# Optimization experiments

Hardware: AMD Instinct MI355X
Metric: run time of the kernel (lower is better)

## Reference

```python
import jax, jax.numpy as jnp
import numpy as np

B, S, D, H = 4, 2048, 512, 8
DEPTH = D // H


def setup_inputs() -> dict:
    key = jax.random.key(0)
    ks = jax.random.split(key, 12)
    s = 0.02
    return {
        "q": jax.random.normal(ks[0], (B, S, D), jnp.float32),
        "k": jax.random.normal(ks[1], (B, S, D), jnp.float32),
        "v": jax.random.normal(ks[2], (B, S, D), jnp.float32),
        "mask": jax.random.randint(ks[3], (B, 1, 1, S), 0, 2, jnp.int32),
        "wq": jax.random.normal(ks[4], (D, D), jnp.float32) * s,
        "bq": jnp.zeros((D,), jnp.float32),
        "wk": jax.random.normal(ks[5], (D, D), jnp.float32) * s,
        "bk": jnp.zeros((D,), jnp.float32),
        "wv": jax.random.normal(ks[6], (D, D), jnp.float32) * s,
        "bv": jnp.zeros((D,), jnp.float32),
        "wo": jax.random.normal(ks[7], (D, D), jnp.float32) * s,
        "bo": jnp.zeros((D,), jnp.float32),
    }


def _split_heads(x):
    # [B,S,D] -> [B,H,S,depth]
    b = x.shape[0]
    return x.reshape(b, -1, H, DEPTH).transpose(0, 2, 1, 3)


def reference(q, k, v, mask, wq, bq, wk, bk, wv, bv, wo, bo):
    qh = _split_heads(q @ wq + bq)
    kh = _split_heads(k @ wk + bk)
    vh = _split_heads(v @ wv + bv)
    scale = 1.0 / jnp.sqrt(jnp.float32(DEPTH))
    logits = jnp.einsum("bhqd,bhkd->bhqk", qh, kh) * scale
    logits = logits + mask.astype(jnp.float32) * -1e9
    attn = jax.nn.softmax(logits, axis=-1)  # [B,H,Sq,Sk]
    out = jnp.einsum("bhqk,bhkd->bhqd", attn, vh)
    out = out.transpose(0, 2, 1, 3).reshape(q.shape[0], -1, D)
    out = out @ wo + bo
    return out, attn
```

## Files before the change

### kernel.cpp

```cpp
#include <hip/hip_runtime.h>

#define B_ 4
#define S_ 2048
#define D_ 512
#define H_ 8
#define DP_ 64
#define NT_ (S_/64)

typedef __attribute__((ext_vector_type(4))) float f32x4;
typedef __attribute__((ext_vector_type(8))) short short8;

__device__ __forceinline__ short f2bf(float f){
  unsigned u = __float_as_uint(f);
  u += 0x7fff + ((u >> 16) & 1);
  return (short)(u >> 16);
}

#define SWZ(r, kb) ((r)*64 + ((kb) ^ (((r)&7)<<3)))

template<int NC>
__device__ __forceinline__ void stage_tile(const short* __restrict__ g, int rowStride,
                                           short* shbase, int w, int l){
  #pragma unroll
  for(int i = 0; i < NC; ++i){
    int byte = (w*NC + i)*1024 + l*16;
    int row = byte >> 7;
    int gs = ((byte >> 4) & 7) ^ (row & 7);
    const short* src = g + (size_t)row*rowStride + gs*8;
    __builtin_amdgcn_global_load_lds((const __attribute__((address_space(1))) void*)src,
        (__attribute__((address_space(3))) void*)(shbase + (w*NC + i)*512), 16, 0, 0);
  }
}

__global__ void k_prep(const float* __restrict__ w0, const float* __restrict__ w1,
                       const float* __restrict__ w2, const float* __restrict__ w3,
                       short* __restrict__ t0, short* __restrict__ t1,
                       short* __restrict__ t2, short* __restrict__ t3){
  __shared__ float t[32][33];
  const float* w = blockIdx.z == 0 ? w0 : blockIdx.z == 1 ? w1 : blockIdx.z == 2 ? w2 : w3;
  short* wt = blockIdx.z == 0 ? t0 : blockIdx.z == 1 ? t1 : blockIdx.z == 2 ? t2 : t3;
  int bx = blockIdx.x * 32, by = blockIdx.y * 32;
  int tx = threadIdx.x, ty = threadIdx.y;
  #pragma unroll
  for(int i = 0; i < 32; i += 8) t[ty + i][tx] = w[(by + ty + i) * D_ + bx + tx];
  __syncthreads();
  #pragma unroll
  for(int i = 0; i < 32; i += 8) wt[(bx + ty + i) * D_ + by + tx] = f2bf(t[tx][ty + i]);
}

__global__ void k_cast(const float* __restrict__ q, const float* __restrict__ k,
                       const float* __restrict__ v, short* __restrict__ dst){
  const float* s = blockIdx.z == 0 ? q : blockIdx.z == 1 ? k : v;
  short* d = dst + (size_t)blockIdx.z * (B_ * S_ * D_);
  int i = blockIdx.x * 256 + threadIdx.x;
  float4 a = ((const float4*)s)[i * 2];
  float4 b = ((const float4*)s)[i * 2 + 1];
  short8 o;
  o[0]=f2bf(a.x); o[1]=f2bf(a.y); o[2]=f2bf(a.z); o[3]=f2bf(a.w);
  o[4]=f2bf(b.x); o[5]=f2bf(b.y); o[6]=f2bf(b.z); o[7]=f2bf(b.w);
  ((short8*)d)[i] = o;
}

__global__ void k_maskbias(const int* __restrict__ mask, float* __restrict__ mb){
  int i = blockIdx.x * 256 + threadIdx.x;
  if(i < B_ * S_) mb[i] = mask[i] ? -1.0e9f : 0.0f;
}

template<int MODE>
__global__ __launch_bounds__(256) void k_gemm(const short* __restrict__ X,
                                              const short* __restrict__ WT,
                                              const float* __restrict__ bias,
                                              void* __restrict__ Outv){
  __shared__ __align__(16) short As[2][4096];
  __shared__ __align__(16) short Bs[2][4096];
  const int t = threadIdx.x;
  const int m0 = blockIdx.x * 64, n0 = blockIdx.y * 64;
  const int l = t & 63, w = t >> 6;
  const int wr = w >> 1, wc = w & 1;
  f32x4 acc[2][2] = {};
  const short* Xb = X + (size_t)m0 * D_;
  const short* Wb = WT + (size_t)n0 * D_;
  stage_tile<2>(Xb, D_, As[0], w, l);
  stage_tile<2>(Wb, D_, Bs[0], w, l);
  __syncthreads();
  for(int kt = 0; kt < D_ / 64; ++kt){
    if(kt + 1 < D_ / 64){
      stage_tile<2>(Xb + (kt + 1) * 64, D_, As[(kt + 1) & 1], w, l);
      stage_tile<2>(Wb + (kt + 1) * 64, D_, Bs[(kt + 1) & 1], w, l);
    }
    const short* Ac = As[kt & 1];
    const short* Bc = Bs[kt & 1];
    #pragma unroll
    for(int ks = 0; ks < 2; ++ks){
      const int kb = ks * 32 + ((l >> 4) << 3);
      short8 a[2], b[2];
      #pragma unroll
      for(int mt = 0; mt < 2; ++mt){
        int r = wr * 32 + mt * 16 + (l & 15);
        a[mt] = *reinterpret_cast<const short8*>(&Ac[SWZ(r, kb)]);
      }
      #pragma unroll
      for(int nt = 0; nt < 2; ++nt){
        int r = wc * 32 + nt * 16 + (l & 15);
        b[nt] = *reinterpret_cast<const short8*>(&Bc[SWZ(r, kb)]);
      }
      __builtin_amdgcn_s_setprio(1);
      #pragma unroll
      for(int mt = 0; mt < 2; ++mt)
        #pragma unroll
        for(int nt = 0; nt < 2; ++nt)
          acc[mt][nt] = __builtin_amdgcn_mfma_f32_16x16x32_bf16(a[mt], b[nt], acc[mt][nt], 0, 0, 0);
      __builtin_amdgcn_s_setprio(0);
    }
    __syncthreads();
  }
  #pragma unroll
  for(int mt = 0; mt < 2; ++mt){
    #pragma unroll
    for(int nt = 0; nt < 2; ++nt){
      const int n = n0 + wc * 32 + nt * 16 + (l & 15);
      const int m4 = m0 + wr * 32 + mt * 16 + ((l >> 4) << 2);
      float vals[4];
      #pragma unroll
      for(int r = 0; r < 4; ++r) vals[r] = acc[mt][nt][r] + bias[n];
      if(MODE == 0){
        #pragma unroll
        for(int r = 0; r < 4; ++r){
          int m = m4 + r;
          ((short*)Outv)[(((size_t)((m >> 11) * H_ + (n >> 6))) * S_ + (m & 2047)) * DP_ + (n & 63)] = f2bf(vals[r]);
        }
      } else if(MODE == 1){
        #pragma unroll
        for(int r = 0; r < 4; ++r)
          ((float*)Outv)[(size_t)(m4 + r) * D_ + n] = vals[r];
      } else {
        short4 pv4;
        pv4.x = f2bf(vals[0]); pv4.y = f2bf(vals[1]); pv4.z = f2bf(vals[2]); pv4.w = f2bf(vals[3]);
        *reinterpret_cast<short4*>(&((short*)Outv)[
            (((size_t)((m4 >> 11) * H_ + (n >> 6))) * DP_ + (n & 63)) * S_ + (m4 & 2047)]) = pv4;
      }
    }
  }
}

__global__ __launch_bounds__(512, 4) void k_attn(const short* __restrict__ qh,
                                                 const short* __restrict__ kh,
                                                 const short* __restrict__ vt,
                                                 const float* __restrict__ mb,
                                                 float* __restrict__ attn,
                                                 short* __restrict__ ctx){
  __shared__ __align__(16) short Sh[24576];
  const int t = threadIdx.x, l = t & 63, w = t >> 6;
  const int lr = l & 15, lg = l >> 4;
  const int bh = blockIdx.y, b = bh >> 3, h = bh & 7;
  const int q0 = blockIdx.x * 128;
  const short* Qb = qh + (size_t)bh * S_ * DP_ + (size_t)q0 * DP_;
  const short* Kb = kh + (size_t)bh * S_ * DP_;
  const short* Vtb = vt + (size_t)bh * DP_ * S_;
  const float* Mbb = mb + b * S_;
  const float scale = 0.125f;

  stage_tile<2>(Qb, DP_, Sh + 16384, w, l);
  stage_tile<1>(Kb, DP_, Sh, w, l);
  __syncthreads();
  short8 bq[2];
  {
    int r = w * 16 + lr;
    #pragma unroll
    for(int ks = 0; ks < 2; ++ks)
      bq[ks] = *reinterpret_cast<const short8*>(&Sh[16384 + SWZ(r, ks * 32 + lg * 8)]);
  }

  float ps = 0.f;
  for(int kt = 0; kt < NT_; ++kt){
    const short* Kc = Sh + (kt & 1) * 4096;
    if(kt + 1 < NT_)
      stage_tile<1>(Kb + (size_t)(kt + 1) * 64 * DP_, DP_, Sh + ((kt + 1) & 1) * 4096, w, l);
    #pragma unroll
    for(int st = 0; st < 4; ++st){
      const float4 mv = *reinterpret_cast<const float4*>(&Mbb[kt * 64 + st * 16 + lg * 4]);
      short8 ak0 = *reinterpret_cast<const short8*>(&Kc[SWZ(st * 16 + lr, lg * 8)]);
      short8 ak1 = *reinterpret_cast<const short8*>(&Kc[SWZ(st * 16 + lr, 32 + lg * 8)]);
      __builtin_amdgcn_s_setprio(1);
      f32x4 c = {};
      c = __builtin_amdgcn_mfma_f32_16x16x32_bf16(ak0, bq[0], c, 0, 0, 0);
      c = __builtin_amdgcn_mfma_f32_16x16x32_bf16(ak1, bq[1], c, 0, 0, 0);
      __builtin_amdgcn_s_setprio(0);
      ps += __expf(__builtin_fmaf(c[0], scale, mv.x));
      ps += __expf(__builtin_fmaf(c[1], scale, mv.y));
      ps += __expf(__builtin_fmaf(c[2], scale, mv.z));
      ps += __expf(__builtin_fmaf(c[3], scale, mv.w));
    }
    __syncthreads();
  }
  ps += __shfl_xor(ps, 16, 64);
  ps += __shfl_xor(ps, 32, 64);
  const float rinv = 1.f / ps;

  f32x4 o[4] = {};
  short* Pw = Sh + 16384 + w * 1024;
  stage_tile<1>(Kb, DP_, Sh, w, l);
  stage_tile<1>(Vtb, S_, Sh + 8192, w, l);
  __syncthreads();
  for(int kt = 0; kt < NT_; ++kt){
    const short* Kc = Sh + (kt & 1) * 4096;
    const short* Vc = Sh + 8192 + (kt & 1) * 4096;
    if(kt + 1 < NT_){
      stage_tile<1>(Kb + (size_t)(kt + 1) * 64 * DP_, DP_, Sh + ((kt + 1) & 1) * 4096, w, l);
      stage_tile<1>(Vtb + (size_t)(kt + 1) * 64, S_, Sh + 8192 + ((kt + 1) & 1) * 4096, w, l);
    }
    #pragma unroll
    for(int st = 0; st < 4; ++st){
      const float4 mv = *reinterpret_cast<const float4*>(&Mbb[kt * 64 + st * 16 + lg * 4]);
      short8 ak0 = *reinterpret_cast<const short8*>(&Kc[SWZ(st * 16 + lr, lg * 8)]);
      short8 ak1 = *reinterpret_cast<const short8*>(&Kc[SWZ(st * 16 + lr, 32 + lg * 8)]);
      __builtin_amdgcn_s_setprio(1);
      f32x4 c = {};
      c = __builtin_amdgcn_mfma_f32_16x16x32_bf16(ak0, bq[0], c, 0, 0, 0);
      c = __builtin_amdgcn_mfma_f32_16x16x32_bf16(ak1, bq[1], c, 0, 0, 0);
      __builtin_amdgcn_s_setprio(0);
      float4 pw;
      pw.x = __expf(__builtin_fmaf(c[0], scale, mv.x)) * rinv;
      pw.y = __expf(__builtin_fmaf(c[1], scale, mv.y)) * rinv;
      pw.z = __expf(__builtin_fmaf(c[2], scale, mv.z)) * rinv;
      pw.w = __expf(__builtin_fmaf(c[3], scale, mv.w)) * rinv;
      const int q = q0 + w * 16 + lr;
      *reinterpret_cast<float4*>(&attn[((size_t)bh * S_ + q) * S_ + kt * 64 + st * 16 + lg * 4]) = pw;
      short4 pb;
      pb.x = f2bf(pw.x); pb.y = f2bf(pw.y); pb.z = f2bf(pw.z); pb.w = f2bf(pw.w);
      *reinterpret_cast<short4*>(&Pw[SWZ(lr, st * 16 + lg * 4)]) = pb;
    }
    #pragma unroll
    for(int ks = 0; ks < 2; ++ks){
      short8 pa = *reinterpret_cast<const short8*>(&Pw[SWZ(lr, ks * 32 + lg * 8)]);
      __builtin_amdgcn_s_setprio(1);
      #pragma unroll
      for(int dt = 0; dt < 4; ++dt){
        short8 vb = *reinterpret_cast<const short8*>(&Vc[SWZ(dt * 16 + lr, ks * 32 + lg * 8)]);
        o[dt] = __builtin_amdgcn_mfma_f32_16x16x32_bf16(pa, vb, o[dt], 0, 0, 0);
      }
      __builtin_amdgcn_s_setprio(0);
    }
    __syncthreads();
  }
  #pragma unroll
  for(int dt = 0; dt < 4; ++dt){
    #pragma unroll
    for(int r = 0; r < 4; ++r){
      int q = q0 + w * 16 + lg * 4 + r;
      int dd = h * 64 + dt * 16 + lr;
      ctx[((size_t)b * S_ + q) * D_ + dd] = f2bf(o[dt][r]);
    }
  }
}

extern "C" void kernel_launch(void* const* d_in, const int* in_sizes, int n_in,
                              void* d_out, int out_size, void* d_ws, size_t ws_size,
                              hipStream_t stream){
  const float* q  = (const float*)d_in[0];
  const float* k  = (const float*)d_in[1];
  const float* v  = (const float*)d_in[2];
  const int* mask = (const int*)d_in[3];
  const float* wq = (const float*)d_in[4];
  const float* bq = (const float*)d_in[5];
  const float* wk = (const float*)d_in[6];
  const float* bk = (const float*)d_in[7];
  const float* wv = (const float*)d_in[8];
  const float* bv = (const float*)d_in[9];
  const float* wo = (const float*)d_in[10];
  const float* bo = (const float*)d_in[11];

  float* out  = (float*)d_out;
  float* attn = out + (size_t)B_ * S_ * D_;

  char* ws = (char*)d_ws;
  short* qkvc = (short*)ws;
  short* qc = qkvc;
  short* kc = qkvc + (size_t)B_ * S_ * D_;
  short* vc = qkvc + (size_t)2 * B_ * S_ * D_;
  short* qh  = (short*)(ws + 25165824);
  short* kh  = (short*)(ws + 33554432);
  short* vvt = (short*)(ws + 41943040);
  short* ctx = (short*)(ws + 50331648);
  short* wqT = (short*)(ws + 58720256);
  short* wkT = (short*)(ws + 58720256 + 524288);
  short* wvT = (short*)(ws + 58720256 + 2 * 524288);
  short* woT = (short*)(ws + 58720256 + 3 * 524288);
  float* mb  = (float*)(ws + 58720256 + 4 * 524288);

  hipLaunchKernelGGL(k_prep, dim3(16, 16, 4), dim3(32, 8), 0, stream,
                     wq, wk, wv, wo, wqT, wkT, wvT, woT);
  hipLaunchKernelGGL(k_cast, dim3(2048, 1, 3), dim3(256), 0, stream, q, k, v, qkvc);
  hipLaunchKernelGGL(k_maskbias, dim3(32), dim3(256), 0, stream, mask, mb);

  dim3 gg(128, 8);
  hipLaunchKernelGGL((k_gemm<0>), gg, dim3(256), 0, stream, qc, wqT, bq, (void*)qh);
  hipLaunchKernelGGL((k_gemm<0>), gg, dim3(256), 0, stream, kc, wkT, bk, (void*)kh);
  hipLaunchKernelGGL((k_gemm<2>), gg, dim3(256), 0, stream, vc, wvT, bv, (void*)vvt);

  hipLaunchKernelGGL(k_attn, dim3(16, 32), dim3(512), 0, stream, qh, kh, vvt, mb, attn, ctx);

  hipLaunchKernelGGL((k_gemm<1>), gg, dim3(256), 0, stream, ctx, woT, bo, (void*)out);
}
```

Baseline: 273.1 us.

## Enlarge GEMM tiles, merge QKV projections, and give attention warps two query tiles

The three QKV projection GEMMs become one launch with a z-dimension, and both the projection and output GEMMs move from 64x64 to 128x128 tiles with a 4x4 MFMA accumulator grid per warp. The attention kernel drops from 512 to 256 threads, and each warp now handles two 16-row query sub-tiles, so every K/V fragment read from LDS feeds twice as many MFMAs. This is meant to raise operand reuse and cut launch count. In exchange it raises register pressure and leaves fewer blocks in flight, which could lower occupancy.

After: 294.0 us. 1.08x slower.

```diff
diff --git a/kernel.cpp b/kernel.cpp
--- a/kernel.cpp
+++ b/kernel.cpp
@@ -18,7 +18,7 @@
 
 #define SWZ(r, kb) ((r)*64 + ((kb) ^ (((r)&7)<<3)))
 
-template<int NC>
+template<int NC, int NW>
 __device__ __forceinline__ void stage_tile(const short* __restrict__ g, int rowStride,
                                            short* shbase, int w, int l){
   #pragma unroll
@@ -66,84 +66,135 @@
   if(i < B_ * S_) mb[i] = mask[i] ? -1.0e9f : 0.0f;
 }
 
-template<int MODE>
-__global__ __launch_bounds__(256) void k_gemm(const short* __restrict__ X,
-                                              const short* __restrict__ WT,
-                                              const float* __restrict__ bias,
-                                              void* __restrict__ Outv){
-  __shared__ __align__(16) short As[2][4096];
-  __shared__ __align__(16) short Bs[2][4096];
-  const int t = threadIdx.x;
-  const int m0 = blockIdx.x * 64, n0 = blockIdx.y * 64;
-  const int l = t & 63, w = t >> 6;
+__global__ __launch_bounds__(256) void k_gemm_qkv(const short* __restrict__ Xall,
+        const short* __restrict__ WTall, const float* __restrict__ b0,
+        const float* __restrict__ b1, const float* __restrict__ b2,
+        short* __restrict__ qh, short* __restrict__ kh, short* __restrict__ vvt){
+  __shared__ __align__(16) short As[2][8192];
+  __shared__ __align__(16) short Bs[2][8192];
+  const int z = blockIdx.z;
+  const short* X  = Xall + (size_t)z * (B_*S_*D_);
+  const short* WT = WTall + (size_t)z * (D_*D_);
+  const float* bias = z==0 ? b0 : (z==1 ? b1 : b2);
+  const int t = threadIdx.x, l = t & 63, w = t >> 6;
+  const int lr = l & 15, lg = l >> 4;
+  const int m0 = blockIdx.x * 128, n0 = blockIdx.y * 128;
   const int wr = w >> 1, wc = w & 1;
-  f32x4 acc[2][2] = {};
   const short* Xb = X + (size_t)m0 * D_;
   const short* Wb = WT + (size_t)n0 * D_;
-  stage_tile<2>(Xb, D_, As[0], w, l);
-  stage_tile<2>(Wb, D_, Bs[0], w, l);
+  f32x4 acc[4][4] = {};
+  stage_tile<4,4>(Xb, D_, As[0], w, l);
+  stage_tile<4,4>(Wb, D_, Bs[0], w, l);
   __syncthreads();
   for(int kt = 0; kt < D_ / 64; ++kt){
     if(kt + 1 < D_ / 64){
-      stage_tile<2>(Xb + (kt + 1) * 64, D_, As[(kt + 1) & 1], w, l);
-      stage_tile<2>(Wb + (kt + 1) * 64, D_, Bs[(kt + 1) & 1], w, l);
-    }
-    const short* Ac = As[kt & 1];
-    const short* Bc = Bs[kt & 1];
+      stage_tile<4,4>(Xb + (kt+1)*64, D_, As[(kt+1)&1], w, l);
+      stage_tile<4,4>(Wb + (kt+1)*64, D_, Bs[(kt+1)&1], w, l);
+    }
+    const short* Ac = As[kt&1];
+    const short* Bc = Bs[kt&1];
     #pragma unroll
     for(int ks = 0; ks < 2; ++ks){
-      const int kb = ks * 32 + ((l >> 4) << 3);
-      short8 a[2], b[2];
-      #pragma unroll
-      for(int mt = 0; mt < 2; ++mt){
-        int r = wr * 32 + mt * 16 + (l & 15);
-        a[mt] = *reinterpret_cast<const short8*>(&Ac[SWZ(r, kb)]);
-      }
-      #pragma unroll
-      for(int nt = 0; nt < 2; ++nt){
-        int r = wc * 32 + nt * 16 + (l & 15);
-        b[nt] = *reinterpret_cast<const short8*>(&Bc[SWZ(r, kb)]);
-      }
+      const int kb = ks*32 + lg*8;
+      short8 a[4], b[4];
+      #pragma unroll
+      for(int mt = 0; mt < 4; ++mt)
+        a[mt] = *reinterpret_cast<const short8*>(&Ac[SWZ(wr*64 + mt*16 + lr, kb)]);
+      #pragma unroll
+      for(int nt = 0; nt < 4; ++nt)
+        b[nt] = *reinterpret_cast<const short8*>(&Bc[SWZ(wc*64 + nt*16 + lr, kb)]);
       __builtin_amdgcn_s_setprio(1);
       #pragma unroll
-      for(int mt = 0; mt < 2; ++mt)
+      for(int mt = 0; mt < 4; ++mt)
         #pragma unroll
-        for(int nt = 0; nt < 2; ++nt)
+        for(int nt = 0; nt < 4; ++nt)
           acc[mt][nt] = __builtin_amdgcn_mfma_f32_16x16x32_bf16(a[mt], b[nt], acc[mt][nt], 0, 0, 0);
       __builtin_amdgcn_s_setprio(0);
     }
     __syncthreads();
   }
   #pragma unroll
-  for(int mt = 0; mt < 2; ++mt){
-    #pragma unroll
-    for(int nt = 0; nt < 2; ++nt){
-      const int n = n0 + wc * 32 + nt * 16 + (l & 15);
-      const int m4 = m0 + wr * 32 + mt * 16 + ((l >> 4) << 2);
+  for(int mt = 0; mt < 4; ++mt){
+    #pragma unroll
+    for(int nt = 0; nt < 4; ++nt){
+      const int n = n0 + wc*64 + nt*16 + lr;
+      const int m4 = m0 + wr*64 + mt*16 + lg*4;
       float vals[4];
       #pragma unroll
       for(int r = 0; r < 4; ++r) vals[r] = acc[mt][nt][r] + bias[n];
-      if(MODE == 0){
+      if(z == 2){
+        short4 pv4;
+        pv4.x = f2bf(vals[0]); pv4.y = f2bf(vals[1]); pv4.z = f2bf(vals[2]); pv4.w = f2bf(vals[3]);
+        *reinterpret_cast<short4*>(&vvt[
+            (((size_t)((m4 >> 11) * H_ + (n >> 6))) * DP_ + (n & 63)) * S_ + (m4 & 2047)]) = pv4;
+      } else {
+        short* dst = z == 0 ? qh : kh;
         #pragma unroll
         for(int r = 0; r < 4; ++r){
           int m = m4 + r;
-          ((short*)Outv)[(((size_t)((m >> 11) * H_ + (n >> 6))) * S_ + (m & 2047)) * DP_ + (n & 63)] = f2bf(vals[r]);
+          dst[(((size_t)((m >> 11) * H_ + (n >> 6))) * S_ + (m & 2047)) * DP_ + (n & 63)] = f2bf(vals[r]);
         }
-      } else if(MODE == 1){
+      }
+    }
+  }
+}
+
+__global__ __launch_bounds__(256) void k_gemm_out(const short* __restrict__ X,
+        const short* __restrict__ WT, const float* __restrict__ bias,
+        float* __restrict__ Out){
+  __shared__ __align__(16) short As[2][8192];
+  __shared__ __align__(16) short Bs[2][8192];
+  const int t = threadIdx.x, l = t & 63, w = t >> 6;
+  const int lr = l & 15, lg = l >> 4;
+  const int m0 = blockIdx.x * 128, n0 = blockIdx.y * 128;
+  const int wr = w >> 1, wc = w & 1;
+  const short* Xb = X + (size_t)m0 * D_;
+  const short* Wb = WT + (size_t)n0 * D_;
+  f32x4 acc[4][4] = {};
+  stage_tile<4,4>(Xb, D_, As[0], w, l);
+  stage_tile<4,4>(Wb, D_, Bs[0], w, l);
+  __syncthreads();
+  for(int kt = 0; kt < D_ / 64; ++kt){
+    if(kt + 1 < D_ / 64){
+      stage_tile<4,4>(Xb + (kt+1)*64, D_, As[(kt+1)&1], w, l);
+      stage_tile<4,4>(Wb + (kt+1)*64, D_, Bs[(kt+1)&1], w, l);
+    }
+    const short* Ac = As[kt&1];
+    const short* Bc = Bs[kt&1];
+    #pragma unroll
+    for(int ks = 0; ks < 2; ++ks){
+      const int kb = ks*32 + lg*8;
+      short8 a[4], b[4];
+      #pragma unroll
+      for(int mt = 0; mt < 4; ++mt)
+        a[mt] = *reinterpret_cast<const short8*>(&Ac[SWZ(wr*64 + mt*16 + lr, kb)]);
+      #pragma unroll
+      for(int nt = 0; nt < 4; ++nt)
+        b[nt] = *reinterpret_cast<const short8*>(&Bc[SWZ(wc*64 + nt*16 + lr, kb)]);
+      __builtin_amdgcn_s_setprio(1);
+      #pragma unroll
+      for(int mt = 0; mt < 4; ++mt)
         #pragma unroll
-        for(int r = 0; r < 4; ++r)
-          ((float*)Outv)[(size_t)(m4 + r) * D_ + n] = vals[r];
-      } else {
-        short4 pv4;
-        pv4.x = f2bf(vals[0]); pv4.y = f2bf(vals[1]); pv4.z = f2bf(vals[2]); pv4.w = f2bf(vals[3]);
-        *reinterpret_cast<short4*>(&((short*)Outv)[
-            (((size_t)((m4 >> 11) * H_ + (n >> 6))) * DP_ + (n & 63)) * S_ + (m4 & 2047)]) = pv4;
-      }
-    }
-  }
-}
-
-__global__ __launch_bounds__(512, 4) void k_attn(const short* __restrict__ qh,
+        for(int nt = 0; nt < 4; ++nt)
+          acc[mt][nt] = __builtin_amdgcn_mfma_f32_16x16x32_bf16(a[mt], b[nt], acc[mt][nt], 0, 0, 0);
+      __builtin_amdgcn_s_setprio(0);
+    }
+    __syncthreads();
+  }
+  #pragma unroll
+  for(int mt = 0; mt < 4; ++mt){
+    #pragma unroll
+    for(int nt = 0; nt < 4; ++nt){
+      const int n = n0 + wc*64 + nt*16 + lr;
+      const int m4 = m0 + wr*64 + mt*16 + lg*4;
+      #pragma unroll
+      for(int r = 0; r < 4; ++r)
+        Out[(size_t)(m4 + r) * D_ + n] = acc[mt][nt][r] + bias[n];
+    }
+  }
+}
+
+__global__ __launch_bounds__(256, 3) void k_attn(const short* __restrict__ qh,
                                                  const short* __restrict__ kh,
                                                  const short* __restrict__ vt,
                                                  const float* __restrict__ mb,
@@ -160,96 +211,112 @@
   const float* Mbb = mb + b * S_;
   const float scale = 0.125f;
 
-  stage_tile<2>(Qb, DP_, Sh + 16384, w, l);
-  stage_tile<1>(Kb, DP_, Sh, w, l);
-  __syncthreads();
-  short8 bq[2];
-  {
-    int r = w * 16 + lr;
+  stage_tile<4,4>(Qb, DP_, Sh + 16384, w, l);
+  stage_tile<2,4>(Kb, DP_, Sh, w, l);
+  __syncthreads();
+  short8 bq[2][2];
+  #pragma unroll
+  for(int qsub = 0; qsub < 2; ++qsub){
+    int r = w * 32 + qsub * 16 + lr;
     #pragma unroll
     for(int ks = 0; ks < 2; ++ks)
-      bq[ks] = *reinterpret_cast<const short8*>(&Sh[16384 + SWZ(r, ks * 32 + lg * 8)]);
-  }
-
-  float ps = 0.f;
+      bq[qsub][ks] = *reinterpret_cast<const short8*>(&Sh[16384 + SWZ(r, ks * 32 + lg * 8)]);
+  }
+
+  float ps[2] = {0.f, 0.f};
   for(int kt = 0; kt < NT_; ++kt){
     const short* Kc = Sh + (kt & 1) * 4096;
     if(kt + 1 < NT_)
-      stage_tile<1>(Kb + (size_t)(kt + 1) * 64 * DP_, DP_, Sh + ((kt + 1) & 1) * 4096, w, l);
+      stage_tile<2,4>(Kb + (size_t)(kt + 1) * 64 * DP_, DP_, Sh + ((kt + 1) & 1) * 4096, w, l);
     #pragma unroll
     for(int st = 0; st < 4; ++st){
       const float4 mv = *reinterpret_cast<const float4*>(&Mbb[kt * 64 + st * 16 + lg * 4]);
       short8 ak0 = *reinterpret_cast<const short8*>(&Kc[SWZ(st * 16 + lr, lg * 8)]);
       short8 ak1 = *reinterpret_cast<const short8*>(&Kc[SWZ(st * 16 + lr, 32 + lg * 8)]);
-      __builtin_amdgcn_s_setprio(1);
-      f32x4 c = {};
-      c = __builtin_amdgcn_mfma_f32_16x16x32_bf16(ak0, bq[0], c, 0, 0, 0);
-      c = __builtin_amdgcn_mfma_f32_16x16x32_bf16(ak1, bq[1], c, 0, 0, 0);
-      __builtin_amdgcn_s_setprio(0);
-      ps += __expf(__builtin_fmaf(c[0], scale, mv.x));
-      ps += __expf(__builtin_fmaf(c[1], scale, mv.y));
-      ps += __expf(__builtin_fmaf(c[2], scale, mv.z));
-      ps += __expf(__builtin_fmaf(c[3], scale, mv.w));
+      #pragma unroll
+      for(int qsub = 0; qsub < 2; ++qsub){
+        __builtin_amdgcn_s_setprio(1);
+        f32x4 c = {};
+        c = __builtin_amdgcn_mfma_f32_16x16x32_bf16(ak0, bq[qsub][0], c, 0, 0, 0);
+        c = __builtin_amdgcn_mfma_f32_16x16x32_bf16(ak1, bq[qsub][1], c, 0, 0, 0);
+        __builtin_amdgcn_s_setprio(0);
+        ps[qsub] += __expf(__builtin_fmaf(c[0], scale, mv.x));
+        ps[qsub] += __expf(__builtin_fmaf(c[1], scale, mv.y));
+        ps[qsub] += __expf(__builtin_fmaf(c[2], scale, mv.z));
+        ps[qsub] += __expf(__builtin_fmaf(c[3], scale, mv.w));
+      }
     }
     __syncthreads();
   }
-  ps += __shfl_xor(ps, 16, 64);
-  ps += __shfl_xor(ps, 32, 64);
-  const float rinv = 1.f / ps;
-
-  f32x4 o[4] = {};
-  short* Pw = Sh + 16384 + w * 1024;
-  stage_tile<1>(Kb, DP_, Sh, w, l);
-  stage_tile<1>(Vtb, S_, Sh + 8192, w, l);
+  #pragma unroll
+  for(int qsub = 0; qsub < 2; ++qsub){
+    ps[qsub] += __shfl_xor(ps[qsub], 16, 64);
+    ps[qsub] += __shfl_xor(ps[qsub], 32, 64);
+  }
+  const float rinv0 = 1.f / ps[0], rinv1 = 1.f / ps[1];
+
+  f32x4 o[2][4] = {};
+  short* Pw = Sh + 16384 + w * 2048;
+  stage_tile<2,4>(Kb, DP_, Sh, w, l);
+  stage_tile<2,4>(Vtb, S_, Sh + 8192, w, l);
   __syncthreads();
   for(int kt = 0; kt < NT_; ++kt){
     const short* Kc = Sh + (kt & 1) * 4096;
     const short* Vc = Sh + 8192 + (kt & 1) * 4096;
     if(kt + 1 < NT_){
-      stage_tile<1>(Kb + (size_t)(kt + 1) * 64 * DP_, DP_, Sh + ((kt + 1) & 1) * 4096, w, l);
-      stage_tile<1>(Vtb + (size_t)(kt + 1) * 64, S_, Sh + 8192 + ((kt + 1) & 1) * 4096, w, l);
+      stage_tile<2,4>(Kb + (size_t)(kt + 1) * 64 * DP_, DP_, Sh + ((kt + 1) & 1) * 4096, w, l);
+      stage_tile<2,4>(Vtb + (size_t)(kt + 1) * 64, S_, Sh + 8192 + ((kt + 1) & 1) * 4096, w, l);
     }
     #pragma unroll
     for(int st = 0; st < 4; ++st){
       const float4 mv = *reinterpret_cast<const float4*>(&Mbb[kt * 64 + st * 16 + lg * 4]);
       short8 ak0 = *reinterpret_cast<const short8*>(&Kc[SWZ(st * 16 + lr, lg * 8)]);
       short8 ak1 = *reinterpret_cast<const short8*>(&Kc[SWZ(st * 16 + lr, 32 + lg * 8)]);
-      __builtin_amdgcn_s_setprio(1);
-      f32x4 c = {};
-      c = __builtin_amdgcn_mfma_f32_16x16x32_bf16(ak0, bq[0], c, 0, 0, 0);
-      c = __builtin_amdgcn_mfma_f32_16x16x32_bf16(ak1, bq[1], c, 0, 0, 0);
-      __builtin_amdgcn_s_setprio(0);
-      float4 pw;
-      pw.x = __expf(__builtin_fmaf(c[0], scale, mv.x)) * rinv;
-      pw.y = __expf(__builtin_fmaf(c[1], scale, mv.y)) * rinv;
-      pw.z = __expf(__builtin_fmaf(c[2], scale, mv.z)) * rinv;
-      pw.w = __expf(__builtin_fmaf(c[3], scale, mv.w)) * rinv;
-      const int q = q0 + w * 16 + lr;
-      *reinterpret_cast<float4*>(&attn[((size_t)bh * S_ + q) * S_ + kt * 64 + st * 16 + lg * 4]) = pw;
-      short4 pb;
-      pb.x = f2bf(pw.x); pb.y = f2bf(pw.y); pb.z = f2bf(pw.z); pb.w = f2bf(pw.w);
-      *reinterpret_cast<short4*>(&Pw[SWZ(lr, st * 16 + lg * 4)]) = pb;
+      #pragma unroll
+      for(int qsub = 0; qsub < 2; ++qsub){
+        const float rinv = qsub ? rinv1 : rinv0;
+        __builtin_amdgcn_s_setprio(1);
+        f32x4 c = {};
+        c = __builtin_amdgcn_mfma_f32_16x16x32_bf16(ak0, bq[qsub][0], c, 0, 0, 0);
+        c = __builtin_amdgcn_mfma_f32_16x16x32_bf16(ak1, bq[qsub][1], c, 0, 0, 0);
+        __builtin_amdgcn_s_setprio(0);
+        float4 pw;
+        pw.x = __expf(__builtin_fmaf(c[0], scale, mv.x)) * rinv;
+        pw.y = __expf(__builtin_fmaf(c[1], scale, mv.y)) * rinv;
+        pw.z = __expf(__builtin_fmaf(c[2], scale, mv.z)) * rinv;
+        pw.w = __expf(__builtin_fmaf(c[3], scale, mv.w)) * rinv;
+        const int q = q0 + w * 32 + qsub * 16 + lr;
+        *reinterpret_cast<float4*>(&attn[((size_t)bh * S_ + q) * S_ + kt * 64 + st * 16 + lg * 4]) = pw;
+        short4 pb;
+        pb.x = f2bf(pw.x); pb.y = f2bf(pw.y); pb.z = f2bf(pw.z); pb.w = f2bf(pw.w);
+        *reinterpret_cast<short4*>(&Pw[SWZ(qsub * 16 + lr, st * 16 + lg * 4)]) = pb;
+      }
     }
     #pragma unroll
     for(int ks = 0; ks < 2; ++ks){
-      short8 pa = *reinterpret_cast<const short8*>(&Pw[SWZ(lr, ks * 32 + lg * 8)]);
+      short8 pa0 = *reinterpret_cast<const short8*>(&Pw[SWZ(lr, ks * 32 + lg * 8)]);
+      short8 pa1 = *reinterpret_cast<const short8*>(&Pw[SWZ(16 + lr, ks * 32 + lg * 8)]);
       __builtin_amdgcn_s_setprio(1);
       #pragma unroll
       for(int dt = 0; dt < 4; ++dt){
         short8 vb = *reinterpret_cast<const short8*>(&Vc[SWZ(dt * 16 + lr, ks * 32 + lg * 8)]);
-        o[dt] = __builtin_amdgcn_mfma_f32_16x16x32_bf16(pa, vb, o[dt], 0, 0, 0);
+        o[0][dt] = __builtin_amdgcn_mfma_f32_16x16x32_bf16(pa0, vb, o[0][dt], 0, 0, 0);
+        o[1][dt] = __builtin_amdgcn_mfma_f32_16x16x32_bf16(pa1, vb, o[1][dt], 0, 0, 0);
       }
       __builtin_amdgcn_s_setprio(0);
     }
     __syncthreads();
   }
   #pragma unroll
-  for(int dt = 0; dt < 4; ++dt){
-    #pragma unroll
-    for(int r = 0; r < 4; ++r){
-      int q = q0 + w * 16 + lg * 4 + r;
-      int dd = h * 64 + dt * 16 + lr;
-      ctx[((size_t)b * S_ + q) * D_ + dd] = f2bf(o[dt][r]);
+  for(int qsub = 0; qsub < 2; ++qsub){
+    #pragma unroll
+    for(int dt = 0; dt < 4; ++dt){
+      #pragma unroll
+      for(int r = 0; r < 4; ++r){
+        int q = q0 + w * 32 + qsub * 16 + lg * 4 + r;
+        int dd = h * 64 + dt * 16 + lr;
+        ctx[((size_t)b * S_ + q) * D_ + dd] = f2bf(o[qsub][dt][r]);
+      }
     }
   }
 }
@@ -275,30 +342,22 @@
 
   char* ws = (char*)d_ws;
   short* qkvc = (short*)ws;
-  short* qc = qkvc;
-  short* kc = qkvc + (size_t)B_ * S_ * D_;
-  short* vc = qkvc + (size_t)2 * B_ * S_ * D_;
   short* qh  = (short*)(ws + 25165824);
   short* kh  = (short*)(ws + 33554432);
   short* vvt = (short*)(ws + 41943040);
   short* ctx = (short*)(ws + 50331648);
-  short* wqT = (short*)(ws + 58720256);
-  short* wkT = (short*)(ws + 58720256 + 524288);
-  short* wvT = (short*)(ws + 58720256 + 2 * 524288);
-  short* woT = (short*)(ws + 58720256 + 3 * 524288);
+  short* wT  = (short*)(ws + 58720256);
   float* mb  = (float*)(ws + 58720256 + 4 * 524288);
 
   hipLaunchKernelGGL(k_prep, dim3(16, 16, 4), dim3(32, 8), 0, stream,
-                     wq, wk, wv, wo, wqT, wkT, wvT, woT);
+                     wq, wk, wv, wo, wT, wT + 262144, wT + 2 * 262144, wT + 3 * 262144);
   hipLaunchKernelGGL(k_cast, dim3(2048, 1, 3), dim3(256), 0, stream, q, k, v, qkvc);
   hipLaunchKernelGGL(k_maskbias, dim3(32), dim3(256), 0, stream, mask, mb);
 
-  dim3 gg(128, 8);
-  hipLaunchKernelGGL((k_gemm<0>), gg, dim3(256), 0, stream, qc, wqT, bq, (void*)qh);
-  hipLaunchKernelGGL((k_gemm<0>), gg, dim3(256), 0, stream, kc, wkT, bk, (void*)kh);
-  hipLaunchKernelGGL((k_gemm<2>), gg, dim3(256), 0, stream, vc, wvT, bv, (void*)vvt);
-
-  hipLaunchKernelGGL(k_attn, dim3(16, 32), dim3(512), 0, stream, qh, kh, vvt, mb, attn, ctx);
-
-  hipLaunchKernelGGL((k_gemm<1>), gg, dim3(256), 0, stream, ctx, woT, bo, (void*)out);
-}
+  hipLaunchKernelGGL(k_gemm_qkv, dim3(64, 4, 3), dim3(256), 0, stream,
+                     qkvc, wT, bq, bk, bv, qh, kh, vvt);
+
+  hipLaunchKernelGGL(k_attn, dim3(16, 32), dim3(256), 0, stream, qh, kh, vvt, mb, attn, ctx);
+
+  hipLaunchKernelGGL(k_gemm_out, dim3(64, 4), dim3(256), 0, stream, ctx, wT + 3 * 262144, bo, out);
+}
```
